# Kernel tuning notes

Measured on AMD Instinct MI355X. Metric: run time of the kernel, lower is better.

Reference implementation:

```python
import jax, jax.numpy as jnp
import numpy as np

TOP_K = 2  # CompleteMOERTDETR default top_k


def setup_inputs() -> dict:
    key = jax.random.key(0)
    ks = jax.random.split(key, 6)
    B, S, D, E, Q, C = 128, 400, 256, 6, 300, 6
    return {
        "features": jax.random.normal(ks[0], (B, S, D), jnp.float32),            # flattened encoder feats
        "W1": jax.random.normal(ks[1], (D, D // 2), jnp.float32) * 0.02,          # Linear(input_dim, input_dim//2)
        "b1": jnp.zeros((D // 2,), jnp.float32),
        "W2": jax.random.normal(ks[2], (D // 2, E), jnp.float32) * 0.02,          # Linear(input_dim//2, num_experts)
        "b2": jnp.zeros((E,), jnp.float32),
        "expert_bboxes": jax.random.uniform(ks[3], (E, B, Q, 4), jnp.float32),    # per-expert pred_boxes
        "expert_class_scores": jax.random.normal(ks[4], (E, B, Q, C), jnp.float32),  # per-expert pred_logits
    }


def reference(features, W1, b1, W2, b2, expert_bboxes, expert_class_scores):
    # Router: Linear -> ReLU -> Linear -> Softmax  (router_net)
    h = jax.nn.relu(features @ W1 + b1)                    # [B,S,D/2]
    expert_logits = jax.nn.softmax(h @ W2 + b2, axis=-1)   # [B,S,E]
    # top-k gating over (already softmaxed) expert logits, then renormalizing softmax
    top_vals, top_idx = jax.lax.top_k(expert_logits, TOP_K)  # [B,S,K]
    routing_weights = jax.nn.softmax(top_vals, axis=-1)       # [B,S,K]

    S = features.shape[1]
    Q = expert_bboxes.shape[2]
    n = min(S, Q)  # combine loop runs over min(seq_len, actual_seq_len); static

    idx = top_idx[:, :n, :]           # [B,n,K]
    w = routing_weights[:, :n, :]     # [B,n,K]

    eb = jnp.transpose(expert_bboxes, (1, 2, 0, 3))        # [B,Q,E,4]
    ec = jnp.transpose(expert_class_scores, (1, 2, 0, 3))  # [B,Q,E,C]

    gb = jnp.take_along_axis(eb[:, :n], idx[..., None], axis=2)  # [B,n,K,4]
    gc = jnp.take_along_axis(ec[:, :n], idx[..., None], axis=2)  # [B,n,K,C]

    cb = jnp.einsum("bnkd,bnk->bnd", gb, w)  # weighted combine of bboxes
    cc = jnp.einsum("bnkc,bnk->bnc", gc, w)  # weighted combine of class scores

    # positions beyond n stay zero (combined_* initialized with zeros_like)
    combined_bboxes = jnp.zeros(eb.shape[:2] + (4,), eb.dtype).at[:, :n].set(cb)
    combined_class_scores = jnp.zeros(ec.shape[:2] + (ec.shape[-1],), ec.dtype).at[:, :n].set(cc)
    return combined_bboxes, combined_class_scores
```

## Files before the change

kernel.cpp:

```cpp
#include <hip/hip_runtime.h>
#include <math.h>

#define NB 128
#define SEQ 400
#define DIN 256
#define HID 128
#define NE 6
#define NQ 300
#define NC 6
#define NROW 300
#define M_TOTAL (NB*NROW)
#define ROWS_BLK 64
#define NBLK (M_TOTAL/ROWS_BLK)
#define KCHUNK 64
#define NCHUNK (DIN/KCHUNK)
#define TAU 2e-4f
#define OUT_BBOX_SZ (NB*NQ*4)
#define BM_WORDS (NBLK*2)
#define FIX_BLOCKS 128
#define FIX_GWAVES (FIX_BLOCKS*16)

#define WS_BM_OFF 65536

using short8 = __attribute__((ext_vector_type(8))) short;
using f32x4  = __attribute__((ext_vector_type(4))) float;

__device__ inline unsigned short bf16_rne(float f) {
    unsigned int u = __float_as_uint(f);
    unsigned int r = (u + 0x7FFFu + ((u >> 16) & 1u)) >> 16;
    return (unsigned short)r;
}

__global__ __launch_bounds__(256)
void moe_prep(const float* __restrict__ W1, unsigned short* __restrict__ w1bf)
{
    int g = blockIdx.x * 256 + threadIdx.x;
    int k = g >> 7;
    int n = g & 127;
    unsigned short h = bf16_rne(W1[k * 128 + n]);
    int c  = k >> 6;
    int k2 = (k & 63) << 1;
    w1bf[(c * 16384 + n * 128 + (k2 ^ ((n & 7) << 4))) >> 1] = h;
}

__global__ __launch_bounds__(256)
void moe_main(const float* __restrict__ features, const float* __restrict__ b1,
              const unsigned short* __restrict__ w1bf, const float* __restrict__ W2,
              const float* __restrict__ b2, const float* __restrict__ ebox,
              const float* __restrict__ ecls, unsigned int* __restrict__ bitmap,
              float* __restrict__ out)
{
    __shared__ __align__(16) char s_raw[34048];
    __shared__ __align__(16) float s_w2[HID * NE];
    __shared__ unsigned int s_flagw[2];

    const int t    = (int)threadIdx.x;
    const int lane = t & 63;
    const int wv   = t >> 6;
    const int row0 = (int)blockIdx.x * ROWS_BLK;
    const int r15  = lane & 15;
    const int kq4  = lane >> 4;

    if (t < 2) s_flagw[t] = 0u;
    for (int i = t; i < HID * NE; i += 256) s_w2[i] = W2[i];

    int  arow[4]; int akq[4]; long fbase[4];
    #pragma unroll
    for (int i = 0; i < 4; ++i) {
        int slot = i * 256 + t;
        int r  = slot >> 4;
        int kq = slot & 15;
        arow[i] = r; akq[i] = kq;
        int rowg = row0 + r;
        int bb = rowg / NROW;
        int ss = rowg - bb * NROW;
        fbase[i] = (long)(bb * SEQ + ss) * DIN;
    }

    f32x4 acc[4][2] = {};

    for (int c = 0; c < NCHUNK; ++c) {
        __syncthreads();
        short8 breg[4];
        const short8* bsrc = (const short8*)(w1bf) + (size_t)c * 1024;
        #pragma unroll
        for (int i = 0; i < 4; ++i) breg[i] = bsrc[i * 256 + t];
        #pragma unroll
        for (int i = 0; i < 4; ++i) {
            float4 v = *(const float4*)(features + fbase[i] + c * KCHUNK + akq[i] * 4);
            unsigned short hx = bf16_rne(v.x), hy = bf16_rne(v.y),
                           hz = bf16_rne(v.z), hw = bf16_rne(v.w);
            float lxf = v.x - __uint_as_float((unsigned int)hx << 16);
            float lyf = v.y - __uint_as_float((unsigned int)hy << 16);
            float lzf = v.z - __uint_as_float((unsigned int)hz << 16);
            float lwf = v.w - __uint_as_float((unsigned int)hw << 16);
            short4 hi4 = make_short4((short)hx, (short)hy, (short)hz, (short)hw);
            short4 lo4 = make_short4((short)bf16_rne(lxf), (short)bf16_rne(lyf),
                                     (short)bf16_rne(lzf), (short)bf16_rne(lwf));
            int off = arow[i] * 128 + ((akq[i] * 8) ^ ((arow[i] & 7) << 4));
            *(short4*)(s_raw + off)        = hi4;
            *(short4*)(s_raw + 8192 + off) = lo4;
        }
        #pragma unroll
        for (int i = 0; i < 4; ++i)
            *((short8*)(s_raw + 16384) + i * 256 + t) = breg[i];
        __syncthreads();

        #pragma unroll
        for (int ks = 0; ks < 2; ++ks) {
            const int kb = ks * 64 + kq4 * 16;
            short8 bf[2];
            #pragma unroll
            for (int nf = 0; nf < 2; ++nf) {
                int n = wv * 32 + nf * 16 + r15;
                bf[nf] = *(const short8*)(s_raw + 16384 + n * 128 + (kb ^ ((n & 7) << 4)));
            }
            #pragma unroll
            for (int mf = 0; mf < 4; ++mf) {
                int row  = mf * 16 + r15;
                int aoff = row * 128 + (kb ^ ((row & 7) << 4));
                short8 ah = *(const short8*)(s_raw + aoff);
                short8 al = *(const short8*)(s_raw + 8192 + aoff);
                #pragma unroll
                for (int nf = 0; nf < 2; ++nf) {
                    acc[mf][nf] = __builtin_amdgcn_mfma_f32_16x16x32_bf16(ah, bf[nf], acc[mf][nf], 0, 0, 0);
                    acc[mf][nf] = __builtin_amdgcn_mfma_f32_16x16x32_bf16(al, bf[nf], acc[mf][nf], 0, 0, 0);
                }
            }
        }
    }

    __syncthreads();
    float* s_h = (float*)s_raw;
    #pragma unroll
    for (int nf = 0; nf < 2; ++nf) {
        int col = wv * 32 + nf * 16 + r15;
        float bias = b1[col];
        #pragma unroll
        for (int mf = 0; mf < 4; ++mf) {
            int row = mf * 16 + kq4 * 4;
            #pragma unroll
            for (int r = 0; r < 4; ++r)
                s_h[(row + r) * 132 + col] = fmaxf(acc[mf][nf][r] + bias, 0.f);
        }
    }
    __syncthreads();

    const int lrow = t >> 2;
    const int part = t & 3;
    float l[6] = {0.f, 0.f, 0.f, 0.f, 0.f, 0.f};
    {
        const float* hp = s_h + lrow * 132 + part * 32;
        const float* wp = s_w2 + part * 32 * NE;
        #pragma unroll
        for (int g = 0; g < 8; ++g) {
            float4 h4 = *(const float4*)(hp + g * 4);
            float w[24];
            #pragma unroll
            for (int q = 0; q < 6; ++q)
                *(float4*)(w + q * 4) = *(const float4*)(wp + g * 24 + q * 4);
            #pragma unroll
            for (int e = 0; e < 6; ++e)
                l[e] += h4.x * w[e] + h4.y * w[6 + e] + h4.z * w[12 + e] + h4.w * w[18 + e];
        }
    }
    #pragma unroll
    for (int e = 0; e < 6; ++e) { l[e] += __shfl_xor(l[e], 1); l[e] += __shfl_xor(l[e], 2); }

    if (part == 0) {
        float lg[NE];
        #pragma unroll
        for (int e = 0; e < NE; ++e) lg[e] = l[e] + b2[e];
        float m = lg[0];
        #pragma unroll
        for (int e = 1; e < NE; ++e) m = fmaxf(m, lg[e]);
        float p[NE]; float psum = 0.f;
        #pragma unroll
        for (int e = 0; e < NE; ++e) { p[e] = expf(lg[e] - m); psum += p[e]; }
        #pragma unroll
        for (int e = 0; e < NE; ++e) p[e] = p[e] / psum;

        int i0 = 0; float v0 = p[0];
        #pragma unroll
        for (int e = 1; e < NE; ++e) if (p[e] > v0) { v0 = p[e]; i0 = e; }
        int i1 = -1; float v1 = -1e38f;
        #pragma unroll
        for (int e = 0; e < NE; ++e) if (e != i0 && p[e] > v1) { v1 = p[e]; i1 = e; }
        float v2 = -1e38f;
        #pragma unroll
        for (int e = 0; e < NE; ++e) if (e != i0 && e != i1 && p[e] > v2) v2 = p[e];

        int rowg = row0 + lrow;
        bool flg = (v1 - v2 < TAU);
        if (flg) atomicOr(&s_flagw[lrow >> 5], 1u << (lrow & 31));

        if (!flg) {
            float e1 = expf(v1 - v0);
            float rw0 = 1.f / (1.f + e1);
            float rw1 = e1 / (1.f + e1);

            int bb = rowg / NROW;
            int ss = rowg - bb * NROW;
            size_t bo0 = ((size_t)(i0 * NB + bb) * NQ + ss) * 4;
            size_t bo1 = ((size_t)(i1 * NB + bb) * NQ + ss) * 4;
            float4 g0 = *(const float4*)(ebox + bo0);
            float4 g1 = *(const float4*)(ebox + bo1);
            float4 ob;
            ob.x = rw0 * g0.x + rw1 * g1.x;
            ob.y = rw0 * g0.y + rw1 * g1.y;
            ob.z = rw0 * g0.z + rw1 * g1.z;
            ob.w = rw0 * g0.w + rw1 * g1.w;
            *(float4*)(out + (size_t)rowg * 4) = ob;

            size_t co0 = ((size_t)(i0 * NB + bb) * NQ + ss) * NC;
            size_t co1 = ((size_t)(i1 * NB + bb) * NQ + ss) * NC;
            float* oc = out + OUT_BBOX_SZ + (size_t)rowg * NC;
            #pragma unroll
            for (int k = 0; k < NC; ++k)
                oc[k] = rw0 * ecls[co0 + k] + rw1 * ecls[co1 + k];
        }
    }

    __syncthreads();
    if (t == 0) {
        bitmap[(size_t)blockIdx.x * 2 + 0] = s_flagw[0];
        bitmap[(size_t)blockIdx.x * 2 + 1] = s_flagw[1];
    }
}

__global__ __launch_bounds__(1024)
void moe_fix(const float* __restrict__ features, const float* __restrict__ W1,
             const float* __restrict__ b1, const float* __restrict__ W2,
             const float* __restrict__ b2, const float* __restrict__ ebox,
             const float* __restrict__ ecls, const unsigned int* __restrict__ bitmap,
             float* __restrict__ out)
{
    __shared__ float s_w1[DIN * HID];
    __shared__ unsigned int s_bm[BM_WORDS];
    __shared__ int s_a[BM_WORDS];
    __shared__ int s_b[BM_WORDS];

    const int t    = (int)threadIdx.x;
    const int lane = t & 63;
    const int gw   = ((int)blockIdx.x << 4) + (t >> 6);

    {
        const float4* src = (const float4*)W1;
        float4* dst = (float4*)s_w1;
        #pragma unroll
        for (int i = 0; i < 8; ++i) dst[i * 1024 + t] = src[i * 1024 + t];
    }
    for (int i = t; i < BM_WORDS; i += 1024) {
        unsigned int w = bitmap[i];
        s_bm[i] = w;
        s_a[i] = (int)__popc(w);
    }
    __syncthreads();

    int* src = s_a; int* dst = s_b;
    for (int s = 1; s < BM_WORDS; s <<= 1) {
        for (int i = t; i < BM_WORDS; i += 1024)
            dst[i] = src[i] + (i >= s ? src[i - s] : 0);
        __syncthreads();
        int* tmp = src; src = dst; dst = tmp;
    }
    const int N = src[BM_WORDS - 1];

    const int c0 = lane * 2;

    for (int o = gw; o < N; o += FIX_GWAVES) {
        int lo = 0, hi = BM_WORDS - 1;
        while (lo < hi) {
            int mid = (lo + hi) >> 1;
            if (src[mid] > o) hi = mid; else lo = mid + 1;
        }
        int excl = lo ? src[lo - 1] : 0;
        int k = o - excl;
        unsigned int w = s_bm[lo];
        for (int j = 0; j < k; ++j) w &= w - 1;
        int row = lo * 32 + (int)__builtin_ctz(w);

        int bb = row / NROW;
        int ss = row - bb * NROW;
        const float* fp = features + (size_t)(bb * SEQ + ss) * DIN;

        float a0 = 0.f, a1 = 0.f;
        #pragma unroll 8
        for (int d = 0; d < DIN; d += 4) {
            float4 f4 = *(const float4*)(fp + d);
            float2 w0 = *(const float2*)(s_w1 + (d + 0) * HID + c0);
            float2 w1 = *(const float2*)(s_w1 + (d + 1) * HID + c0);
            float2 w2 = *(const float2*)(s_w1 + (d + 2) * HID + c0);
            float2 w3 = *(const float2*)(s_w1 + (d + 3) * HID + c0);
            a0 = fmaf(f4.x, w0.x, a0); a1 = fmaf(f4.x, w0.y, a1);
            a0 = fmaf(f4.y, w1.x, a0); a1 = fmaf(f4.y, w1.y, a1);
            a0 = fmaf(f4.z, w2.x, a0); a1 = fmaf(f4.z, w2.y, a1);
            a0 = fmaf(f4.w, w3.x, a0); a1 = fmaf(f4.w, w3.y, a1);
        }
        float h0 = fmaxf(a0 + b1[c0], 0.f);
        float h1 = fmaxf(a1 + b1[c0 + 1], 0.f);

        float lg[NE];
        #pragma unroll
        for (int e = 0; e < NE; ++e) {
            float v = h0 * W2[c0 * NE + e] + h1 * W2[(c0 + 1) * NE + e];
            #pragma unroll
            for (int off = 1; off < 64; off <<= 1) v += __shfl_xor(v, off);
            lg[e] = v + b2[e];
        }
        float mx = lg[0];
        #pragma unroll
        for (int e = 1; e < NE; ++e) mx = fmaxf(mx, lg[e]);
        float pr[NE]; float psum = 0.f;
        #pragma unroll
        for (int e = 0; e < NE; ++e) { pr[e] = expf(lg[e] - mx); psum += pr[e]; }
        #pragma unroll
        for (int e = 0; e < NE; ++e) pr[e] = pr[e] / psum;

        int i0 = 0; float v0 = pr[0];
        #pragma unroll
        for (int e = 1; e < NE; ++e) if (pr[e] > v0) { v0 = pr[e]; i0 = e; }
        int i1 = -1; float v1 = -1e38f;
        #pragma unroll
        for (int e = 0; e < NE; ++e) if (e != i0 && pr[e] > v1) { v1 = pr[e]; i1 = e; }

        if (lane == 0) {
            float e1 = expf(v1 - v0);
            float rw0 = 1.f / (1.f + e1);
            float rw1 = e1 / (1.f + e1);
            size_t bo0 = ((size_t)(i0 * NB + bb) * NQ + ss) * 4;
            size_t bo1 = ((size_t)(i1 * NB + bb) * NQ + ss) * 4;
            float4 g0 = *(const float4*)(ebox + bo0);
            float4 g1 = *(const float4*)(ebox + bo1);
            float4 ob;
            ob.x = rw0 * g0.x + rw1 * g1.x;
            ob.y = rw0 * g0.y + rw1 * g1.y;
            ob.z = rw0 * g0.z + rw1 * g1.z;
            ob.w = rw0 * g0.w + rw1 * g1.w;
            *(float4*)(out + (size_t)row * 4) = ob;
            size_t co0 = ((size_t)(i0 * NB + bb) * NQ + ss) * NC;
            size_t co1 = ((size_t)(i1 * NB + bb) * NQ + ss) * NC;
            float* oc = out + OUT_BBOX_SZ + (size_t)row * NC;
            #pragma unroll
            for (int kk = 0; kk < NC; ++kk)
                oc[kk] = rw0 * ecls[co0 + kk] + rw1 * ecls[co1 + kk];
        }
    }
}

extern "C" void kernel_launch(void* const* d_in, const int* in_sizes, int n_in,
                              void* d_out, int out_size, void* d_ws, size_t ws_size,
                              hipStream_t stream)
{
    const float* features = (const float*)d_in[0];
    const float* W1   = (const float*)d_in[1];
    const float* b1   = (const float*)d_in[2];
    const float* W2   = (const float*)d_in[3];
    const float* b2   = (const float*)d_in[4];
    const float* ebox = (const float*)d_in[5];
    const float* ecls = (const float*)d_in[6];
    float* out = (float*)d_out;

    unsigned short* w1bf   = (unsigned short*)d_ws;
    unsigned int*   bitmap = (unsigned int*)((char*)d_ws + WS_BM_OFF);

    hipLaunchKernelGGL(moe_prep, dim3(128), dim3(256), 0, stream, W1, w1bf);
    hipLaunchKernelGGL(moe_main, dim3(NBLK), dim3(256), 0, stream,
                       features, b1, w1bf, W2, b2, ebox, ecls, bitmap, out);
    hipLaunchKernelGGL(moe_fix, dim3(FIX_BLOCKS), dim3(1024), 0, stream,
                       features, W1, b1, W2, b2, ebox, ecls, bitmap, out);
}
```

Before: 43.93 us.

## Use split-bf16 W1 with third MFMA term and tighten fix threshold

The prep kernel now splits W1 into hi and lo bf16 parts, stored in MFMA fragment order, so the main kernel can load B fragments straight from global memory into registers. This removes the LDS staging of W1. A third MFMA (A_hi x B_lo) is added for higher GEMM accuracy, which permits a tighter tolerance (TAU) for the near-tie fallback pass. The aim is to reduce how many rows the expensive fix kernel must recompute, at the cost of 50% more MFMA work and per-wave global loads of B.

```diff
diff --git a/kernel.cpp b/kernel.cpp
--- a/kernel.cpp
+++ b/kernel.cpp
@@ -14,13 +14,14 @@
 #define NBLK (M_TOTAL/ROWS_BLK)
 #define KCHUNK 64
 #define NCHUNK (DIN/KCHUNK)
-#define TAU 2e-4f
+#define TAU 5e-5f
 #define OUT_BBOX_SZ (NB*NQ*4)
 #define BM_WORDS (NBLK*2)
 #define FIX_BLOCKS 128
 #define FIX_GWAVES (FIX_BLOCKS*16)
 
-#define WS_BM_OFF 65536
+#define WS_LO_OFF 65536
+#define WS_BM_OFF 131072
 
 using short8 = __attribute__((ext_vector_type(8))) short;
 using f32x4  = __attribute__((ext_vector_type(4))) float;
@@ -35,12 +36,25 @@
 void moe_prep(const float* __restrict__ W1, unsigned short* __restrict__ w1bf)
 {
     int g = blockIdx.x * 256 + threadIdx.x;
-    int k = g >> 7;
-    int n = g & 127;
-    unsigned short h = bf16_rne(W1[k * 128 + n]);
-    int c  = k >> 6;
-    int k2 = (k & 63) << 1;
-    w1bf[(c * 16384 + n * 128 + (k2 ^ ((n & 7) << 4))) >> 1] = h;
+    int frag = g >> 6;
+    int lane = g & 63;
+    int nf = frag & 1;
+    int wv = (frag >> 1) & 3;
+    int ks = (frag >> 3) & 1;
+    int c  = frag >> 4;
+    int n  = wv * 32 + nf * 16 + (lane & 15);
+    int k0 = c * 64 + ks * 32 + (lane >> 4) * 8;
+
+    short8 h8, l8;
+    #pragma unroll
+    for (int j = 0; j < 8; ++j) {
+        float v = W1[(size_t)(k0 + j) * HID + n];
+        unsigned short h = bf16_rne(v);
+        h8[j] = (short)h;
+        l8[j] = (short)bf16_rne(v - __uint_as_float((unsigned int)h << 16));
+    }
+    *(short8*)(w1bf + (size_t)frag * 512 + lane * 8)         = h8;
+    *(short8*)(w1bf + 32768 + (size_t)frag * 512 + lane * 8) = l8;
 }
 
 __global__ __launch_bounds__(256)
@@ -60,6 +74,7 @@
     const int row0 = (int)blockIdx.x * ROWS_BLK;
     const int r15  = lane & 15;
     const int kq4  = lane >> 4;
+    const char* w1b = (const char*)w1bf;
 
     if (t < 2) s_flagw[t] = 0u;
     for (int i = t; i < HID * NE; i += 256) s_w2[i] = W2[i];
@@ -80,11 +95,16 @@
     f32x4 acc[4][2] = {};
 
     for (int c = 0; c < NCHUNK; ++c) {
+        short8 bh[2][2], bl[2][2];
+        #pragma unroll
+        for (int ks = 0; ks < 2; ++ks)
+            #pragma unroll
+            for (int nf = 0; nf < 2; ++nf) {
+                size_t base = (size_t)(c * 16 + ks * 8 + wv * 2 + nf) * 1024 + lane * 16;
+                bh[ks][nf] = *(const short8*)(w1b + base);
+                bl[ks][nf] = *(const short8*)(w1b + WS_LO_OFF + base);
+            }
         __syncthreads();
-        short8 breg[4];
-        const short8* bsrc = (const short8*)(w1bf) + (size_t)c * 1024;
-        #pragma unroll
-        for (int i = 0; i < 4; ++i) breg[i] = bsrc[i * 256 + t];
         #pragma unroll
         for (int i = 0; i < 4; ++i) {
             float4 v = *(const float4*)(features + fbase[i] + c * KCHUNK + akq[i] * 4);
@@ -101,20 +121,11 @@
             *(short4*)(s_raw + off)        = hi4;
             *(short4*)(s_raw + 8192 + off) = lo4;
         }
-        #pragma unroll
-        for (int i = 0; i < 4; ++i)
-            *((short8*)(s_raw + 16384) + i * 256 + t) = breg[i];
         __syncthreads();
 
         #pragma unroll
         for (int ks = 0; ks < 2; ++ks) {
             const int kb = ks * 64 + kq4 * 16;
-            short8 bf[2];
-            #pragma unroll
-            for (int nf = 0; nf < 2; ++nf) {
-                int n = wv * 32 + nf * 16 + r15;
-                bf[nf] = *(const short8*)(s_raw + 16384 + n * 128 + (kb ^ ((n & 7) << 4)));
-            }
             #pragma unroll
             for (int mf = 0; mf < 4; ++mf) {
                 int row  = mf * 16 + r15;
@@ -123,8 +134,9 @@
                 short8 al = *(const short8*)(s_raw + 8192 + aoff);
                 #pragma unroll
                 for (int nf = 0; nf < 2; ++nf) {
-                    acc[mf][nf] = __builtin_amdgcn_mfma_f32_16x16x32_bf16(ah, bf[nf], acc[mf][nf], 0, 0, 0);
-                    acc[mf][nf] = __builtin_amdgcn_mfma_f32_16x16x32_bf16(al, bf[nf], acc[mf][nf], 0, 0, 0);
+                    acc[mf][nf] = __builtin_amdgcn_mfma_f32_16x16x32_bf16(ah, bh[ks][nf], acc[mf][nf], 0, 0, 0);
+                    acc[mf][nf] = __builtin_amdgcn_mfma_f32_16x16x32_bf16(al, bh[ks][nf], acc[mf][nf], 0, 0, 0);
+                    acc[mf][nf] = __builtin_amdgcn_mfma_f32_16x16x32_bf16(ah, bl[ks][nf], acc[mf][nf], 0, 0, 0);
                 }
             }
         }
@@ -364,7 +376,7 @@
     unsigned short* w1bf   = (unsigned short*)d_ws;
     unsigned int*   bitmap = (unsigned int*)((char*)d_ws + WS_BM_OFF);
 
-    hipLaunchKernelGGL(moe_prep, dim3(128), dim3(256), 0, stream, W1, w1bf);
+    hipLaunchKernelGGL(moe_prep, dim3(16), dim3(256), 0, stream, W1, w1bf);
     hipLaunchKernelGGL(moe_main, dim3(NBLK), dim3(256), 0, stream,
                        features, b1, w1bf, W2, b2, ebox, ecls, bitmap, out);
     hipLaunchKernelGGL(moe_fix, dim3(FIX_BLOCKS), dim3(1024), 0, stream,
```

Result: no change. 44.16 us (+0.5%).
